# Optimization experiments

Measured on AMD Instinct MI355X. Metric: run time of the kernel, lower is better.

The kernel has to match this reference:

```python
import jax, jax.numpy as jnp
import numpy as np

B, C, H, W = 16, 256, 64, 64
HID, N, SD, NH, HD, NC = 256, 300, 64, 4, 16, 80


def _conv1x1(x, w, b):
    # x: (B,Cin,H,W), w: (Cout,Cin)
    return jnp.einsum('bchw,oc->bohw', x, w) + b[None, :, None, None]


def _lin(x, w, b):
    return x @ w.T + b


def _ln(x, g, b, eps=1e-5):
    mu = x.mean(-1, keepdims=True)
    var = ((x - mu) ** 2).mean(-1, keepdims=True)
    return (x - mu) / jnp.sqrt(var + eps) * g + b


def setup_inputs() -> dict:
    key = jax.random.key(0)
    ks = jax.random.split(key, 16)
    def w(k, shape, s=0.02):
        return jax.random.normal(k, shape, jnp.float32) * s
    return {
        'x': jax.random.normal(ks[0], (B, C, H, W), jnp.float32),
        'spotlight_sources': w(ks[1], (N, SD)),
        'pos_w': w(ks[2], (HID // 2, 2)), 'pos_b': jnp.zeros((HID // 2,), jnp.float32),
        'fp_w': w(ks[3], (HID, C)), 'fp_b': jnp.zeros((HID,), jnp.float32),
        'bn_g': jnp.ones((HID,), jnp.float32), 'bn_b': jnp.zeros((HID,), jnp.float32),
        'bn_m': jnp.zeros((HID,), jnp.float32), 'bn_v': jnp.ones((HID,), jnp.float32),
        'key_w': w(ks[4], (SD, HID)), 'key_b': jnp.zeros((SD,), jnp.float32),
        'val_w': w(ks[5], (HID, HID)), 'val_b': jnp.zeros((HID,), jnp.float32),
        'ctp_w': w(ks[6], (NC, HID)), 'ctp_b': jnp.zeros((NC,), jnp.float32),
        'bb1_w': w(ks[7], (HID, HID)), 'bb1_b': jnp.zeros((HID,), jnp.float32),
        'bbln_g': jnp.ones((HID,), jnp.float32), 'bbln_b': jnp.zeros((HID,), jnp.float32),
        'bb2_w': w(ks[8], (HID // 2, HID)), 'bb2_b': jnp.zeros((HID // 2,), jnp.float32),
        'bb3_w': w(ks[9], (4, HID // 2)), 'bb3_b': jnp.zeros((4,), jnp.float32),
        'ch1_w': w(ks[10], (HID, HID)), 'ch1_b': jnp.zeros((HID,), jnp.float32),
        'chln_g': jnp.ones((HID,), jnp.float32), 'chln_b': jnp.zeros((HID,), jnp.float32),
        'ch2_w': w(ks[11], (HID // 2, HID)), 'ch2_b': jnp.zeros((HID // 2,), jnp.float32),
        'ch3_w': w(ks[12], (1, HID // 2)), 'ch3_b': jnp.zeros((1,), jnp.float32),
    }


def _forward(x, spotlight_sources, pos_w, pos_b, fp_w, fp_b, bn_g, bn_b, bn_m, bn_v,
             key_w, key_b, val_w, val_b, ctp_w, ctp_b,
             bb1_w, bb1_b, bbln_g, bbln_b, bb2_w, bb2_b, bb3_w, bb3_b,
             ch1_w, ch1_b, chln_g, chln_b, ch2_w, ch2_b, ch3_w, ch3_b):
    Bv, _, Hh, Ww = x.shape
    # position encoding: 2-channel normalized (y, x) grid, conv1x1 to HID//2
    y = jnp.linspace(-1.0, 1.0, Hh, dtype=jnp.float32)
    xc = jnp.linspace(-1.0, 1.0, Ww, dtype=jnp.float32)
    coords = jnp.stack([jnp.broadcast_to(y[:, None], (Hh, Ww)),
                        jnp.broadcast_to(xc[None, :], (Hh, Ww))], 0)[None]  # (1,2,H,W)
    # feature_proj: conv1x1 + BatchNorm(eval) + ReLU
    feats = _conv1x1(x, fp_w, fp_b)
    feats = (feats - bn_m[None, :, None, None]) / jnp.sqrt(bn_v[None, :, None, None] + 1e-5)
    feats = jax.nn.relu(feats * bn_g[None, :, None, None] + bn_b[None, :, None, None])
    pos = jnp.broadcast_to(_conv1x1(coords, pos_w, pos_b), (Bv, HID // 2, Hh, Ww))
    comb = jnp.concatenate([feats[:, :HID // 2], pos], axis=1)  # (B,HID,H,W)
    keys = _conv1x1(comb, key_w, key_b).reshape(Bv, NH, HD, Hh * Ww)   # (B,h,d,M)
    vals = _conv1x1(comb, val_w, val_b).reshape(Bv, HID, Hh * Ww)      # (B,HID,M)
    q = spotlight_sources.reshape(N, NH, HD)                            # (N,h,d)
    logits = jnp.einsum('nhd,bhdm->bhnm', q, keys) / jnp.sqrt(jnp.float32(HD))
    attn = jax.nn.softmax(logits, axis=-1).mean(axis=1)                 # (B,N,M), head-averaged
    maps = attn.reshape(Bv, N, Hh, Ww)
    sf = jnp.einsum('bnm,bcm->bnc', attn, vals)                         # (B,N,HID)
    def head(z, w1, b1, g, bb, w2, b2, w3, b3):
        z = jax.nn.relu(_ln(_lin(z, w1, b1), g, bb))
        z = jax.nn.relu(_lin(z, w2, b2))
        return _lin(z, w3, b3)
    boxes = head(sf, bb1_w, bb1_b, bbln_g, bbln_b, bb2_w, bb2_b, bb3_w, bb3_b)
    scores = jax.nn.sigmoid(head(sf, ch1_w, ch1_b, chln_g, chln_b, ch2_w, ch2_b, ch3_w, ch3_b))
    cls = _lin(sf, ctp_w, ctp_b)
    # diversity loss: mean off-diagonal cosine similarity of attention rows
    an = attn / jnp.maximum(jnp.linalg.norm(attn, axis=2, keepdims=True), 1e-12)
    sim = jnp.einsum('bnm,bkm->bnk', an, an)
    div = (sim.sum() - jnp.einsum('bnn->', sim)) / (N * (N - 1)) * 0.1
    return boxes, scores, cls, maps, div, sf


def reference(x, spotlight_sources, pos_w, pos_b, fp_w, fp_b, bn_g, bn_b, bn_m, bn_v,
              key_w, key_b, val_w, val_b, ctp_w, ctp_b,
              bb1_w, bb1_b, bbln_g, bbln_b, bb2_w, bb2_b, bb3_w, bb3_b,
              ch1_w, ch1_b, chln_g, chln_b, ch2_w, ch2_b, ch3_w, ch3_b):
    return _forward(x, spotlight_sources, pos_w, pos_b, fp_w, fp_b, bn_g, bn_b, bn_m, bn_v,
                    key_w, key_b, val_w, val_b, ctp_w, ctp_b,
                    bb1_w, bb1_b, bbln_g, bbln_b, bb2_w, bb2_b, bb3_w, bb3_b,
                    ch1_w, ch1_b, chln_g, chln_b, ch2_w, ch2_b, ch3_w, ch3_b)
```

## Files before the change

kernel.cpp:

```cpp
#include <hip/hip_runtime.h>
#include <math.h>

#define BB 16
#define CIN 256
#define MM 4096
#define HIDC 256
#define NQ 300
#define NHH 4
#define HDD 16

#define OFF_BOXES  0
#define OFF_SCORES 19200
#define OFF_CLS    24000
#define OFF_MAPS   408000
#define OFF_DIV    20068800
#define OFF_SF     20068801

#define WS_COMB16  0
#define WS_KEYS16  8388608
#define WS_ATTN16  10485760
#define WS_T32     20316160
#define WS_T16     21544960
#define WS_VALW16  22159360
#define WS_SUMS    22192128
#define WS_NORM    22211328
#define WS_ACC     22216128
#define WS_P       22216192

#define HP_SF16   (WS_P + 0)
#define HP_Z1PRE  (WS_P + 614400)
#define HP_Z1_16  (WS_P + 1843200)
#define HP_Z2BB   (WS_P + 2457600)
#define HP_Z2CH   (WS_P + 2764800)
#define HP_HW     (WS_P + 3072000)
#define WS_Q16    (WS_P + 3200000)
#define WS_XT     25426432
#define WS_COMBT  33815040
#define WS_FPW16  42203648
#define WS_KEYW16 42220032

#define HW_BB1 0
#define HW_CH1 65536
#define HW_BB2 131072
#define HW_CH2 163840
#define HW_CTP 196608

typedef short short8 __attribute__((ext_vector_type(8)));
typedef float floatx4 __attribute__((ext_vector_type(4)));

__device__ __forceinline__ unsigned short f2bf(float f){
  unsigned int u = __float_as_uint(f);
  u = (u + 0x7FFFu + ((u >> 16) & 1u)) >> 16;
  return (unsigned short)u;
}
__device__ __forceinline__ float bf1(unsigned short u){
  return __uint_as_float((unsigned int)u << 16);
}

__global__ void zero_kernel(float* p){ p[0] = 0.f; }

__global__ __launch_bounds__(256) void zero4_kernel(float4* __restrict__ p, int n4){
  int i = blockIdx.x * 256 + threadIdx.x;
  if (i < n4) p[i] = make_float4(0.f, 0.f, 0.f, 0.f);
}

__global__ __launch_bounds__(256) void cast4_bf16_kernel(const float* __restrict__ src,
                                                         unsigned short* __restrict__ dst, int n4){
  int i = blockIdx.x * 256 + threadIdx.x;
  if (i < n4){
    float4 v = ((const float4*)src)[i];
    ushort4 u;
    u.x = f2bf(v.x); u.y = f2bf(v.y); u.z = f2bf(v.z); u.w = f2bf(v.w);
    ((ushort4*)dst)[i] = u;
  }
}

__global__ __launch_bounds__(256) void castq_kernel(const float* __restrict__ ss,
                                                    unsigned short* __restrict__ q16){
  int i = blockIdx.x * 256 + threadIdx.x;
  if (i < 320*64)
    q16[i] = (i < NQ*64) ? f2bf(ss[i] * 0.25f) : (unsigned short)0;
}

__global__ __launch_bounds__(256) void cast_w2_kernel(const float* __restrict__ fp_w,
    const float* __restrict__ key_w,
    unsigned short* __restrict__ fpw16, unsigned short* __restrict__ keyw16){
  int i = blockIdx.x * 256 + threadIdx.x;
  if (i < 128*256) fpw16[i] = f2bf(fp_w[i]);
  if (i < 64*256)  keyw16[i] = f2bf(key_w[i]);
}

__global__ __launch_bounds__(256) void cast_heads_kernel(
    const float* __restrict__ val_w, const float* __restrict__ bb1_w,
    const float* __restrict__ ch1_w, const float* __restrict__ bb2_w,
    const float* __restrict__ ch2_w, const float* __restrict__ ctp_w,
    unsigned short* __restrict__ valw16, unsigned short* __restrict__ hw16){
  int i = blockIdx.x * 256 + threadIdx.x;
  int T = gridDim.x * 256;
  for (int j = i; j < 65536; j += T) valw16[j] = f2bf(val_w[j]);
  for (int j = i; j < 65536; j += T) hw16[HW_BB1 + j] = f2bf(bb1_w[j]);
  for (int j = i; j < 65536; j += T) hw16[HW_CH1 + j] = f2bf(ch1_w[j]);
  for (int j = i; j < 32768; j += T) hw16[HW_BB2 + j] = f2bf(bb2_w[j]);
  for (int j = i; j < 32768; j += T) hw16[HW_CH2 + j] = f2bf(ch2_w[j]);
  for (int j = i; j < 20480; j += T) hw16[HW_CTP + j] = f2bf(ctp_w[j]);
}

__global__ __launch_bounds__(256) void pos_fill_kernel(const float* __restrict__ pos_w,
                                                       const float* __restrict__ pos_b,
                                                       unsigned short* __restrict__ comb16){
  int idx = blockIdx.x * 256 + threadIdx.x;
  int c = idx >> 12;
  int m = idx & 4095;
  int row = m >> 6, col = m & 63;
  float y = -1.f + 2.f * (float)row / 63.f;
  float x = -1.f + 2.f * (float)col / 63.f;
  unsigned short v = f2bf(pos_w[c*2] * y + pos_w[c*2+1] * x + pos_b[c]);
  #pragma unroll
  for (int b = 0; b < BB; b++)
    comb16[((size_t)(b*HIDC + 128 + c))*MM + m] = v;
}

template<bool INF32>
__global__ __launch_bounds__(256) void transpose_kernel(
    const void* __restrict__ in, unsigned short* __restrict__ outp){
  int b = blockIdx.z;
  int m0 = blockIdx.x * 64;
  int r0 = blockIdx.y * 64;
  __shared__ unsigned short lds[64][65];
  int t = threadIdx.x;
  if (INF32){
    const float* ib = (const float*)in + (size_t)b * CIN * MM;
    #pragma unroll
    for (int j = 0; j < 4; j++){
      int lin = j*256 + t;
      int rr = lin >> 4;
      int m4 = (lin & 15) * 4;
      float4 v = *(const float4*)&ib[(size_t)(r0 + rr)*MM + m0 + m4];
      lds[m4+0][rr] = f2bf(v.x);
      lds[m4+1][rr] = f2bf(v.y);
      lds[m4+2][rr] = f2bf(v.z);
      lds[m4+3][rr] = f2bf(v.w);
    }
  } else {
    const unsigned short* ib = (const unsigned short*)in + (size_t)b * CIN * MM;
    #pragma unroll
    for (int j = 0; j < 4; j++){
      int lin = j*256 + t;
      int rr = lin >> 4;
      int m4 = (lin & 15) * 4;
      ushort4 v = *(const ushort4*)&ib[(size_t)(r0 + rr)*MM + m0 + m4];
      lds[m4+0][rr] = v.x; lds[m4+1][rr] = v.y;
      lds[m4+2][rr] = v.z; lds[m4+3][rr] = v.w;
    }
  }
  __syncthreads();
  unsigned short* ob = outp + (size_t)b * MM * CIN;
  #pragma unroll
  for (int j = 0; j < 4; j++){
    int lin = j*256 + t;
    int mm = lin >> 4;
    int c4 = (lin & 15) * 4;
    ushort4 u;
    u.x = lds[mm][c4+0]; u.y = lds[mm][c4+1];
    u.z = lds[mm][c4+2]; u.w = lds[mm][c4+3];
    *(ushort4*)&ob[(size_t)(m0 + mm)*CIN + r0 + c4] = u;
  }
}

__global__ __launch_bounds__(64) void comb_mfma_kernel(
    const unsigned short* __restrict__ fpw16, const unsigned short* __restrict__ xT16,
    const float* __restrict__ fp_b, const float* __restrict__ bn_g,
    const float* __restrict__ bn_b, const float* __restrict__ bn_m,
    const float* __restrict__ bn_v, unsigned short* __restrict__ comb16){
  int b = blockIdx.z;
  const unsigned short* Bb = xT16 + (size_t)b * MM * CIN;
  unsigned short* cb = comb16 + (size_t)b * HIDC * MM;
  int lane = threadIdx.x;
  int r16 = lane & 15;
  int ko  = (lane >> 4) * 8;
  const unsigned short* arow[4];
  const unsigned short* brow[4];
  #pragma unroll
  for (int i = 0; i < 4; i++){
    arow[i] = fpw16 + (size_t)(blockIdx.y*64 + i*16 + r16) * CIN + ko;
    brow[i] = Bb + (size_t)(blockIdx.x*64 + i*16 + r16) * CIN + ko;
  }
  floatx4 acc[4][4];
  #pragma unroll
  for (int i = 0; i < 4; i++)
    #pragma unroll
    for (int j = 0; j < 4; j++)
      acc[i][j] = (floatx4){0.f, 0.f, 0.f, 0.f};
  short8 a[4], bv[4], a2[4], b2[4];
  #pragma unroll
  for (int i = 0; i < 4; i++){
    a[i]  = *(const short8*)(arow[i]);
    bv[i] = *(const short8*)(brow[i]);
  }
  for (int k = 32; k < CIN; k += 32){
    #pragma unroll
    for (int i = 0; i < 4; i++){
      a2[i] = *(const short8*)(arow[i] + k);
      b2[i] = *(const short8*)(brow[i] + k);
    }
    #pragma unroll
    for (int i = 0; i < 4; i++)
      #pragma unroll
      for (int j = 0; j < 4; j++)
        acc[i][j] = __builtin_amdgcn_mfma_f32_16x16x32_bf16(a[i], bv[j], acc[i][j], 0, 0, 0);
    #pragma unroll
    for (int i = 0; i < 4; i++){ a[i] = a2[i]; bv[i] = b2[i]; }
  }
  #pragma unroll
  for (int i = 0; i < 4; i++)
    #pragma unroll
    for (int j = 0; j < 4; j++)
      acc[i][j] = __builtin_amdgcn_mfma_f32_16x16x32_bf16(a[i], bv[j], acc[i][j], 0, 0, 0);
  int cq = lane & 15, rq = (lane >> 4) * 4;
  #pragma unroll
  for (int i = 0; i < 4; i++){
    #pragma unroll
    for (int reg = 0; reg < 4; reg++){
      int rr = blockIdx.y*64 + i*16 + rq + reg;
      float sc  = rsqrtf(bn_v[rr] + 1e-5f);
      float mul = sc * bn_g[rr];
      float ofs = (fp_b[rr] - bn_m[rr]) * mul + bn_b[rr];
      #pragma unroll
      for (int j = 0; j < 4; j++){
        int cc = blockIdx.x*64 + j*16 + cq;
        float v = fmaxf(acc[i][j][reg] * mul + ofs, 0.f);
        cb[(size_t)rr * MM + cc] = f2bf(v);
      }
    }
  }
}


__global__ __launch_bounds__(256) void attn_sums_kernel(
    const unsigned short* __restrict__ q16, const unsigned short* __restrict__ keysT,
    float* __restrict__ sums){
  int b = blockIdx.z, ny = blockIdx.y, mx = blockIdx.x;
  int tid = threadIdx.x, w = tid >> 6, lane = tid & 63;
  int n0 = ny * 64;
  int l15 = lane & 15, qh = lane >> 4;
  int ko = (qh & 1) * 8;
  bool lo = lane < 32;
  const unsigned short* kT = keysT + (size_t)b * MM * 64;
  int mwb = mx*512 + w*128;
  __shared__ float spart[4][NHH][64];
  short8 zz = {0,0,0,0,0,0,0,0};
  for (int h = 0; h < NHH; h++){
    short8 a[4];
    #pragma unroll
    for (int i = 0; i < 4; i++)
      a[i] = lo ? *(const short8*)&q16[(size_t)(n0 + i*16 + l15)*64 + h*16 + ko] : zz;
    floatx4 sacc[4];
    #pragma unroll
    for (int i = 0; i < 4; i++) sacc[i] = (floatx4){0.f,0.f,0.f,0.f};
    for (int ms = 0; ms < 8; ms++){
      int m = mwb + ms*16 + l15;
      short8 bf = lo ? *(const short8*)&kT[(size_t)m*64 + h*16 + ko] : zz;
      #pragma unroll
      for (int i = 0; i < 4; i++){
        floatx4 l = __builtin_amdgcn_mfma_f32_16x16x32_bf16(a[i], bf,
                        (floatx4){0.f,0.f,0.f,0.f}, 0, 0, 0);
        sacc[i][0] += __expf(l[0]); sacc[i][1] += __expf(l[1]);
        sacc[i][2] += __expf(l[2]); sacc[i][3] += __expf(l[3]);
      }
    }
    #pragma unroll
    for (int i = 0; i < 4; i++)
      #pragma unroll
      for (int reg = 0; reg < 4; reg++){
        float v = sacc[i][reg];
        v += __shfl_xor(v, 1); v += __shfl_xor(v, 2);
        v += __shfl_xor(v, 4); v += __shfl_xor(v, 8);
        if (l15 == 0) spart[w][h][i*16 + qh*4 + reg] = v;
      }
  }
  __syncthreads();
  if (tid < NHH*64){
    int h = tid >> 6, r = tid & 63, n = n0 + r;
    if (n < NQ){
      float v = spart[0][h][r] + spart[1][h][r] + spart[2][h][r] + spart[3][h][r];
      atomicAdd(&sums[((size_t)b*NHH + h)*NQ + n], v);
    }
  }
}

__global__ __launch_bounds__(256) void attn_emit_kernel(
    const unsigned short* __restrict__ q16, const unsigned short* __restrict__ keysT,
    const float* __restrict__ sums, float* __restrict__ maps,
    unsigned short* __restrict__ attn16, float* __restrict__ norms){
  int b = blockIdx.z, ny = blockIdx.y, mx = blockIdx.x;
  int tid = threadIdx.x, w = tid >> 6, lane = tid & 63;
  int n0 = ny * 64;
  int l15 = lane & 15, qh = lane >> 4;
  int ko = (qh & 1) * 8;
  int rq = qh * 4;
  bool lo = lane < 32;
  __shared__ __align__(16) float inv_s[NHH][64];
  __shared__ float npart[4][64];
  if (tid < NHH*64){
    int h = tid >> 6, r = tid & 63, n = n0 + r;
    inv_s[h][r] = (n < NQ) ? 0.25f / sums[((size_t)b*NHH + h)*NQ + n] : 0.f;
  }
  __syncthreads();
  const unsigned short* kT = keysT + (size_t)b * MM * 64;
  int mwb = mx*512 + w*128;
  short8 zz = {0,0,0,0,0,0,0,0};
  short8 a[NHH][4];
  #pragma unroll
  for (int h = 0; h < NHH; h++)
    #pragma unroll
    for (int i = 0; i < 4; i++)
      a[h][i] = lo ? *(const short8*)&q16[(size_t)(n0 + i*16 + l15)*64 + h*16 + ko] : zz;
  floatx4 nacc[4];
  #pragma unroll
  for (int i = 0; i < 4; i++) nacc[i] = (floatx4){0.f,0.f,0.f,0.f};
  float* mb = maps + (size_t)b * NQ * MM;
  unsigned short* ab = attn16 + (size_t)b * NQ * MM;
  for (int ms = 0; ms < 8; ms++){
    int m = mwb + ms*16 + l15;
    floatx4 o[4];
    #pragma unroll
    for (int i = 0; i < 4; i++) o[i] = (floatx4){0.f,0.f,0.f,0.f};
    #pragma unroll
    for (int h = 0; h < NHH; h++){
      short8 bf = lo ? *(const short8*)&kT[(size_t)m*64 + h*16 + ko] : zz;
      #pragma unroll
      for (int i = 0; i < 4; i++){
        floatx4 l = __builtin_amdgcn_mfma_f32_16x16x32_bf16(a[h][i], bf,
                        (floatx4){0.f,0.f,0.f,0.f}, 0, 0, 0);
        floatx4 iv = *(const floatx4*)&inv_s[h][i*16 + rq];
        o[i][0] += __expf(l[0]) * iv[0];
        o[i][1] += __expf(l[1]) * iv[1];
        o[i][2] += __expf(l[2]) * iv[2];
        o[i][3] += __expf(l[3]) * iv[3];
      }
    }
    #pragma unroll
    for (int i = 0; i < 4; i++){
      nacc[i][0] += o[i][0]*o[i][0]; nacc[i][1] += o[i][1]*o[i][1];
      nacc[i][2] += o[i][2]*o[i][2]; nacc[i][3] += o[i][3]*o[i][3];
      #pragma unroll
      for (int reg = 0; reg < 4; reg++){
        int n = n0 + i*16 + rq + reg;
        if (n < NQ){
          mb[(size_t)n*MM + m] = o[i][reg];
          ab[(size_t)n*MM + m] = f2bf(o[i][reg]);
        }
      }
    }
  }
  #pragma unroll
  for (int i = 0; i < 4; i++)
    #pragma unroll
    for (int reg = 0; reg < 4; reg++){
      float v = nacc[i][reg];
      v += __shfl_xor(v, 1); v += __shfl_xor(v, 2);
      v += __shfl_xor(v, 4); v += __shfl_xor(v, 8);
      if (l15 == 0) npart[w][i*16 + rq + reg] = v;
    }
  __syncthreads();
  if (tid < 64){
    int n = n0 + tid;
    if (n < NQ){
      float v = npart[0][tid] + npart[1][tid] + npart[2][tid] + npart[3][tid];
      atomicAdd(&norms[(size_t)b*NQ + n], v);
    }
  }
}

template<bool RELU>
__global__ __launch_bounds__(64) void mfma_nt_kernel(
    const unsigned short* __restrict__ A, size_t sA,
    const unsigned short* __restrict__ B, size_t sB,
    const float* __restrict__ bias,
    float* __restrict__ C, unsigned short* __restrict__ C16,
    size_t sC, int ldc, int Mr, int Nc, int K){
  int bz = blockIdx.z;
  const unsigned short* Ab = A + (size_t)bz * sA;
  const unsigned short* Bb = B + (size_t)bz * sB;
  int lane = threadIdx.x;
  int r16 = lane & 15;
  int ko  = (lane >> 4) * 8;
  const unsigned short* arow[4];
  const unsigned short* brow[4];
  #pragma unroll
  for (int i = 0; i < 4; i++){
    int m = blockIdx.y*64 + i*16 + r16;
    if (m > Mr - 1) m = Mr - 1;
    arow[i] = Ab + (size_t)m * K + ko;
    int n = blockIdx.x*64 + i*16 + r16;
    if (n > Nc - 1) n = Nc - 1;
    brow[i] = Bb + (size_t)n * K + ko;
  }
  floatx4 acc[4][4];
  #pragma unroll
  for (int i = 0; i < 4; i++)
    #pragma unroll
    for (int j = 0; j < 4; j++)
      acc[i][j] = (floatx4){0.f, 0.f, 0.f, 0.f};
  short8 a[4], bv[4], a2[4], b2[4];
  #pragma unroll
  for (int i = 0; i < 4; i++){
    a[i]  = *(const short8*)(arow[i]);
    bv[i] = *(const short8*)(brow[i]);
  }
  for (int k = 32; k < K; k += 32){
    #pragma unroll
    for (int i = 0; i < 4; i++){
      a2[i] = *(const short8*)(arow[i] + k);
      b2[i] = *(const short8*)(brow[i] + k);
    }
    #pragma unroll
    for (int i = 0; i < 4; i++)
      #pragma unroll
      for (int j = 0; j < 4; j++)
        acc[i][j] = __builtin_amdgcn_mfma_f32_16x16x32_bf16(a[i], bv[j], acc[i][j], 0, 0, 0);
    #pragma unroll
    for (int i = 0; i < 4; i++){ a[i] = a2[i]; bv[i] = b2[i]; }
  }
  #pragma unroll
  for (int i = 0; i < 4; i++)
    #pragma unroll
    for (int j = 0; j < 4; j++)
      acc[i][j] = __builtin_amdgcn_mfma_f32_16x16x32_bf16(a[i], bv[j], acc[i][j], 0, 0, 0);
  int cq = lane & 15, rq = (lane >> 4) * 4;
  #pragma unroll
  for (int j = 0; j < 4; j++){
    int cc = blockIdx.x*64 + j*16 + cq;
    if (cc >= Nc) continue;
    float bv_ = bias ? bias[cc] : 0.f;
    #pragma unroll
    for (int i = 0; i < 4; i++){
      int rbase = blockIdx.y*64 + i*16 + rq;
      #pragma unroll
      for (int reg = 0; reg < 4; reg++){
        int rr = rbase + reg;
        if (rr < Mr){
          float v = acc[i][j][reg] + bv_;
          if (RELU) v = fmaxf(v, 0.f);
          size_t o = (size_t)bz * sC + (size_t)rr * ldc + cc;
          if (C)   C[o] = v;
          if (C16) C16[o] = f2bf(v);
        }
      }
    }
  }
}

__global__ __launch_bounds__(64) void mfma_nt_splitk_kernel(
    const unsigned short* __restrict__ A, size_t sA,
    const unsigned short* __restrict__ B, size_t sB,
    float* __restrict__ C, size_t sC, int ldc, int Mr, int K, int kchunk){
  int nks = K / kchunk;
  int bz = blockIdx.z / nks;
  int kz = blockIdx.z % nks;
  const unsigned short* Ab = A + (size_t)bz * sA + (size_t)kz * kchunk;
  const unsigned short* Bb = B + (size_t)bz * sB + (size_t)kz * kchunk;
  int lane = threadIdx.x;
  int r16 = lane & 15;
  int ko  = (lane >> 4) * 8;
  const unsigned short* arow[4];
  const unsigned short* brow[4];
  #pragma unroll
  for (int i = 0; i < 4; i++){
    int m = blockIdx.y*64 + i*16 + r16;
    if (m > Mr - 1) m = Mr - 1;
    arow[i] = Ab + (size_t)m * K + ko;
    int n = blockIdx.x*64 + i*16 + r16;
    brow[i] = Bb + (size_t)n * K + ko;
  }
  floatx4 acc[4][4];
  #pragma unroll
  for (int i = 0; i < 4; i++)
    #pragma unroll
    for (int j = 0; j < 4; j++)
      acc[i][j] = (floatx4){0.f, 0.f, 0.f, 0.f};
  short8 a[4], bv[4], a2[4], b2[4];
  #pragma unroll
  for (int i = 0; i < 4; i++){
    a[i]  = *(const short8*)(arow[i]);
    bv[i] = *(const short8*)(brow[i]);
  }
  for (int k = 32; k < kchunk; k += 32){
    #pragma unroll
    for (int i = 0; i < 4; i++){
      a2[i] = *(const short8*)(arow[i] + k);
      b2[i] = *(const short8*)(brow[i] + k);
    }
    #pragma unroll
    for (int i = 0; i < 4; i++)
      #pragma unroll
      for (int j = 0; j < 4; j++)
        acc[i][j] = __builtin_amdgcn_mfma_f32_16x16x32_bf16(a[i], bv[j], acc[i][j], 0, 0, 0);
    #pragma unroll
    for (int i = 0; i < 4; i++){ a[i] = a2[i]; bv[i] = b2[i]; }
  }
  #pragma unroll
  for (int i = 0; i < 4; i++)
    #pragma unroll
    for (int j = 0; j < 4; j++)
      acc[i][j] = __builtin_amdgcn_mfma_f32_16x16x32_bf16(a[i], bv[j], acc[i][j], 0, 0, 0);
  int cq = lane & 15, rq = (lane >> 4) * 4;
  #pragma unroll
  for (int j = 0; j < 4; j++){
    int cc = blockIdx.x*64 + j*16 + cq;
    #pragma unroll
    for (int i = 0; i < 4; i++){
      int rbase = blockIdx.y*64 + i*16 + rq;
      #pragma unroll
      for (int reg = 0; reg < 4; reg++){
        int rr = rbase + reg;
        if (rr < Mr)
          atomicAdd(&C[(size_t)bz * sC + (size_t)rr * ldc + cc], acc[i][j][reg]);
      }
    }
  }
}

__global__ __launch_bounds__(256) void ln_relu_kernel(const float* __restrict__ zin,
    const float* __restrict__ g, const float* __restrict__ bvec,
    unsigned short* __restrict__ zout){
  int row = blockIdx.x * 4 + (threadIdx.x >> 6);
  int lane = threadIdx.x & 63;
  float4 v = *(const float4*)&zin[(size_t)row * 256 + lane * 4];
  float s = v.x + v.y + v.z + v.w;
  #pragma unroll
  for (int off = 32; off >= 1; off >>= 1) s += __shfl_xor(s, off);
  float mean = s * (1.f/256.f);
  float dx = v.x - mean, dy = v.y - mean, dz = v.z - mean, dw = v.w - mean;
  float sq = dx*dx + dy*dy + dz*dz + dw*dw;
  #pragma unroll
  for (int off = 32; off >= 1; off >>= 1) sq += __shfl_xor(sq, off);
  float inv = rsqrtf(sq * (1.f/256.f) + 1e-5f);
  float4 gv = *(const float4*)&g[lane * 4];
  float4 bb = *(const float4*)&bvec[lane * 4];
  ushort4 u;
  u.x = f2bf(fmaxf(dx*inv*gv.x + bb.x, 0.f));
  u.y = f2bf(fmaxf(dy*inv*gv.y + bb.y, 0.f));
  u.z = f2bf(fmaxf(dz*inv*gv.z + bb.z, 0.f));
  u.w = f2bf(fmaxf(dw*inv*gv.w + bb.w, 0.f));
  *(ushort4*)&zout[(size_t)row * 256 + lane * 4] = u;
}

__global__ __launch_bounds__(256) void head3_kernel(
    const unsigned short* __restrict__ z2bb, const unsigned short* __restrict__ z2ch,
    const float* __restrict__ bb3_w, const float* __restrict__ bb3_b,
    const float* __restrict__ ch3_w, const float* __restrict__ ch3_b,
    float* __restrict__ boxes, float* __restrict__ scores){
  int row = blockIdx.x * 4 + (threadIdx.x >> 6);
  int lane = threadIdx.x & 63;
  float zb0 = bf1(z2bb[(size_t)row*128 + 2*lane]);
  float zb1 = bf1(z2bb[(size_t)row*128 + 2*lane + 1]);
  float zc0 = bf1(z2ch[(size_t)row*128 + 2*lane]);
  float zc1 = bf1(z2ch[(size_t)row*128 + 2*lane + 1]);
  float acc[5];
  #pragma unroll
  for (int o = 0; o < 4; o++)
    acc[o] = bb3_w[o*128 + 2*lane]*zb0 + bb3_w[o*128 + 2*lane + 1]*zb1;
  acc[4] = ch3_w[2*lane]*zc0 + ch3_w[2*lane + 1]*zc1;
  #pragma unroll
  for (int o = 0; o < 5; o++){
    float v = acc[o];
    #pragma unroll
    for (int off = 32; off >= 1; off >>= 1) v += __shfl_xor(v, off);
    acc[o] = v;
  }
  if (lane == 0){
    #pragma unroll
    for (int o = 0; o < 4; o++)
      boxes[(size_t)row*4 + o] = acc[o] + bb3_b[o];
    float sv = acc[4] + ch3_b[0];
    scores[row] = 1.f / (1.f + __expf(-sv));
  }
}

__global__ __launch_bounds__(256) void simdiv_kernel(const unsigned short* __restrict__ attn16,
    const float* __restrict__ norms, float* __restrict__ acc){
  int b = blockIdx.y;
  int m = blockIdx.x * 256 + threadIdx.x;
  __shared__ float inv_s[NQ];
  __shared__ float red[4];
  for (int i = threadIdx.x; i < NQ; i += 256)
    inv_s[i] = 1.f / fmaxf(sqrtf(norms[(size_t)b * NQ + i]), 1e-12f);
  __syncthreads();
  const unsigned short* ab = attn16 + (size_t)b * NQ * MM;
  float S = 0.f;
  for (int n = 0; n < NQ; n++)
    S += bf1(ab[(size_t)n * MM + m]) * inv_s[n];
  float p = S * S;
  #pragma unroll
  for (int off = 32; off >= 1; off >>= 1) p += __shfl_xor(p, off);
  int w = threadIdx.x >> 6, lane = threadIdx.x & 63;
  if (lane == 0) red[w] = p;
  __syncthreads();
  if (threadIdx.x == 0) atomicAdd(acc, red[0] + red[1] + red[2] + red[3]);
}

__global__ void finalize_kernel(const float* __restrict__ acc, float* __restrict__ out_div){
  out_div[0] = (acc[0] - (float)(BB * NQ)) / (float)(NQ * (NQ - 1)) * 0.1f;
}

extern "C" void kernel_launch(void* const* d_in, const int* in_sizes, int n_in,
                              void* d_out, int out_size, void* d_ws, size_t ws_size,
                              hipStream_t stream){
  const float* x      = (const float*)d_in[0];
  const float* ss     = (const float*)d_in[1];
  const float* pos_w  = (const float*)d_in[2];
  const float* pos_b  = (const float*)d_in[3];
  const float* fp_w   = (const float*)d_in[4];
  const float* fp_b   = (const float*)d_in[5];
  const float* bn_g   = (const float*)d_in[6];
  const float* bn_b   = (const float*)d_in[7];
  const float* bn_m   = (const float*)d_in[8];
  const float* bn_v   = (const float*)d_in[9];
  const float* key_w  = (const float*)d_in[10];
  const float* key_b  = (const float*)d_in[11];
  const float* val_w  = (const float*)d_in[12];
  const float* val_b  = (const float*)d_in[13];
  const float* ctp_w  = (const float*)d_in[14];
  const float* ctp_b  = (const float*)d_in[15];
  const float* bb1_w  = (const float*)d_in[16];
  const float* bb1_b  = (const float*)d_in[17];
  const float* bbln_g = (const float*)d_in[18];
  const float* bbln_b = (const float*)d_in[19];
  const float* bb2_w  = (const float*)d_in[20];
  const float* bb2_b  = (const float*)d_in[21];
  const float* bb3_w  = (const float*)d_in[22];
  const float* bb3_b  = (const float*)d_in[23];
  const float* ch1_w  = (const float*)d_in[24];
  const float* ch1_b  = (const float*)d_in[25];
  const float* chln_g = (const float*)d_in[26];
  const float* chln_b = (const float*)d_in[27];
  const float* ch2_w  = (const float*)d_in[28];
  const float* ch2_b  = (const float*)d_in[29];
  const float* ch3_w  = (const float*)d_in[30];
  const float* ch3_b  = (const float*)d_in[31];

  float* out    = (float*)d_out;
  float* boxes  = out + OFF_BOXES;
  float* scores = out + OFF_SCORES;
  float* cls    = out + OFF_CLS;
  float* maps   = out + OFF_MAPS;
  float* divp   = out + OFF_DIV;
  float* sfout  = out + OFF_SF;

  float* ws = (float*)d_ws;
  unsigned short* comb16 = (unsigned short*)(ws + WS_COMB16);
  unsigned short* keysT  = (unsigned short*)(ws + WS_KEYS16);
  unsigned short* attn16 = (unsigned short*)(ws + WS_ATTN16);
  float*          t32    = ws + WS_T32;
  unsigned short* t16    = (unsigned short*)(ws + WS_T16);
  unsigned short* valw16 = (unsigned short*)(ws + WS_VALW16);
  float* sums  = ws + WS_SUMS;
  float* norms = ws + WS_NORM;
  float* dacc  = ws + WS_ACC;
  unsigned short* sf16   = (unsigned short*)(ws + HP_SF16);
  float*          z1pre  = ws + HP_Z1PRE;
  unsigned short* z1_16  = (unsigned short*)(ws + HP_Z1_16);
  unsigned short* z2bb16 = (unsigned short*)(ws + HP_Z2BB);
  unsigned short* z2ch16 = (unsigned short*)(ws + HP_Z2CH);
  unsigned short* hw16   = (unsigned short*)(ws + HP_HW);
  unsigned short* q16    = (unsigned short*)(ws + WS_Q16);
  unsigned short* xT16   = (unsigned short*)(ws + WS_XT);
  unsigned short* combT  = (unsigned short*)(ws + WS_COMBT);
  unsigned short* fpw16  = (unsigned short*)(ws + WS_FPW16);
  unsigned short* keyw16 = (unsigned short*)(ws + WS_KEYW16);

  zero_kernel<<<1, 1, 0, stream>>>(dacc);
  zero4_kernel<<<1200, 256, 0, stream>>>((float4*)t32, 307200);
  zero4_kernel<<<24, 256, 0, stream>>>((float4*)sums, 6000);
  castq_kernel<<<80, 256, 0, stream>>>(ss, q16);
  cast_w2_kernel<<<128, 256, 0, stream>>>(fp_w, key_w, fpw16, keyw16);

  transpose_kernel<true><<<dim3(64,4,16), 256, 0, stream>>>(x, xT16);
  pos_fill_kernel<<<2048, 256, 0, stream>>>(pos_w, pos_b, comb16);
  comb_mfma_kernel<<<dim3(64,2,16), 64, 0, stream>>>(
      fpw16, xT16, fp_b, bn_g, bn_b, bn_m, bn_v, comb16);
  transpose_kernel<false><<<dim3(64,4,16), 256, 0, stream>>>(comb16, combT);
  mfma_nt_kernel<false><<<dim3(1,64,16), 64, 0, stream>>>(
      combT, (size_t)MM*CIN, keyw16, 0, key_b,
      nullptr, keysT, (size_t)MM*64, 64, MM, 64, CIN);

  attn_sums_kernel<<<dim3(8,5,16), 256, 0, stream>>>(q16, keysT, sums);
  attn_emit_kernel<<<dim3(8,5,16), 256, 0, stream>>>(q16, keysT, sums, maps, attn16, norms);

  mfma_nt_splitk_kernel<<<dim3(4,5,BB*4), 64, 0, stream>>>(
      attn16, (size_t)NQ*MM, comb16, (size_t)HIDC*MM,
      t32, (size_t)NQ*HIDC, HIDC, NQ, MM, MM/4);
  cast4_bf16_kernel<<<1200, 256, 0, stream>>>(t32, t16, 307200);
  cast_heads_kernel<<<256, 256, 0, stream>>>(val_w, bb1_w, ch1_w, bb2_w, ch2_w, ctp_w, valw16, hw16);
  mfma_nt_kernel<false><<<dim3(4,5,BB), 64, 0, stream>>>(
      t16, (size_t)NQ*HIDC, valw16, 0, val_b,
      sfout, sf16, (size_t)NQ*HIDC, HIDC, NQ, HIDC, HIDC);

  mfma_nt_kernel<false><<<dim3(4,75,1), 64, 0, stream>>>(
      sf16, 0, hw16 + HW_BB1, 0, bb1_b, z1pre, nullptr, 0, 256, 4800, 256, 256);
  ln_relu_kernel<<<1200, 256, 0, stream>>>(z1pre, bbln_g, bbln_b, z1_16);
  mfma_nt_kernel<true><<<dim3(2,75,1), 64, 0, stream>>>(
      z1_16, 0, hw16 + HW_BB2, 0, bb2_b, nullptr, z2bb16, 0, 128, 4800, 128, 256);
  mfma_nt_kernel<false><<<dim3(4,75,1), 64, 0, stream>>>(
      sf16, 0, hw16 + HW_CH1, 0, ch1_b, z1pre, nullptr, 0, 256, 4800, 256, 256);
  ln_relu_kernel<<<1200, 256, 0, stream>>>(z1pre, chln_g, chln_b, z1_16);
  mfma_nt_kernel<true><<<dim3(2,75,1), 64, 0, stream>>>(
      z1_16, 0, hw16 + HW_CH2, 0, ch2_b, nullptr, z2ch16, 0, 128, 4800, 128, 256);
  head3_kernel<<<1200, 256, 0, stream>>>(z2bb16, z2ch16, bb3_w, bb3_b, ch3_w, ch3_b, boxes, scores);
  mfma_nt_kernel<false><<<dim3(2,75,1), 64, 0, stream>>>(
      sf16, 0, hw16 + HW_CTP, 0, ctp_b, cls, nullptr, 0, 80, 4800, 80, 256);

  simdiv_kernel<<<dim3(16,16), 256, 0, stream>>>(attn16, norms, dacc);
  finalize_kernel<<<1, 1, 0, stream>>>(dacc, divp);
}
```

Measured before the change: 565.2 us.

## Coalesce attention map stores via LDS staging, write positional channels transposed directly

The attention emit kernel now stages each 64x16 tile of outputs in shared memory and writes maps and attn16 as float4/ushort4 rows instead of scattered scalar stores. The positional-embedding half of the transposed combined features is filled directly by a new kernel, so the comb transpose only covers the first 128 channels. Both attention kernels use a finer split over positions (twice as many blocks, with the position loop unrolled) for more parallelism, and the transpose LDS row padding changes. The trade-offs are extra LDS use and a barrier-free staging step per wave, plus one extra kernel launch.

```diff
diff --git a/kernel.cpp b/kernel.cpp
--- a/kernel.cpp
+++ b/kernel.cpp
@@ -120,13 +120,32 @@
     comb16[((size_t)(b*HIDC + 128 + c))*MM + m] = v;
 }
 
+__global__ __launch_bounds__(256) void pos_fillT_kernel(const float* __restrict__ pos_w,
+                                                        const float* __restrict__ pos_b,
+                                                        unsigned short* __restrict__ combT){
+  int lin = blockIdx.x * 256 + threadIdx.x;
+  int c4 = (lin & 31) * 4;
+  int m  = lin >> 5;
+  int row = m >> 6, col = m & 63;
+  float y = -1.f + 2.f * (float)row / 63.f;
+  float x = -1.f + 2.f * (float)col / 63.f;
+  ushort4 u;
+  u.x = f2bf(pos_w[(c4+0)*2] * y + pos_w[(c4+0)*2+1] * x + pos_b[c4+0]);
+  u.y = f2bf(pos_w[(c4+1)*2] * y + pos_w[(c4+1)*2+1] * x + pos_b[c4+1]);
+  u.z = f2bf(pos_w[(c4+2)*2] * y + pos_w[(c4+2)*2+1] * x + pos_b[c4+2]);
+  u.w = f2bf(pos_w[(c4+3)*2] * y + pos_w[(c4+3)*2+1] * x + pos_b[c4+3]);
+  #pragma unroll
+  for (int b = 0; b < BB; b++)
+    *(ushort4*)&combT[((size_t)b*MM + m)*CIN + 128 + c4] = u;
+}
+
 template<bool INF32>
 __global__ __launch_bounds__(256) void transpose_kernel(
     const void* __restrict__ in, unsigned short* __restrict__ outp){
   int b = blockIdx.z;
   int m0 = blockIdx.x * 64;
   int r0 = blockIdx.y * 64;
-  __shared__ unsigned short lds[64][65];
+  __shared__ unsigned short lds[64][68];
   int t = threadIdx.x;
   if (INF32){
     const float* ib = (const float*)in + (size_t)b * CIN * MM;
@@ -246,7 +265,7 @@
   int ko = (qh & 1) * 8;
   bool lo = lane < 32;
   const unsigned short* kT = keysT + (size_t)b * MM * 64;
-  int mwb = mx*512 + w*128;
+  int mwb = mx*256 + w*64;
   __shared__ float spart[4][NHH][64];
   short8 zz = {0,0,0,0,0,0,0,0};
   for (int h = 0; h < NHH; h++){
@@ -257,7 +276,8 @@
     floatx4 sacc[4];
     #pragma unroll
     for (int i = 0; i < 4; i++) sacc[i] = (floatx4){0.f,0.f,0.f,0.f};
-    for (int ms = 0; ms < 8; ms++){
+    #pragma unroll
+    for (int ms = 0; ms < 4; ms++){
       int m = mwb + ms*16 + l15;
       short8 bf = lo ? *(const short8*)&kT[(size_t)m*64 + h*16 + ko] : zz;
       #pragma unroll
@@ -301,13 +321,14 @@
   bool lo = lane < 32;
   __shared__ __align__(16) float inv_s[NHH][64];
   __shared__ float npart[4][64];
+  __shared__ __align__(16) float tbuf[4][64][20];
   if (tid < NHH*64){
     int h = tid >> 6, r = tid & 63, n = n0 + r;
     inv_s[h][r] = (n < NQ) ? 0.25f / sums[((size_t)b*NHH + h)*NQ + n] : 0.f;
   }
   __syncthreads();
   const unsigned short* kT = keysT + (size_t)b * MM * 64;
-  int mwb = mx*512 + w*128;
+  int mwb = mx*256 + w*64;
   short8 zz = {0,0,0,0,0,0,0,0};
   short8 a[NHH][4];
   #pragma unroll
@@ -320,8 +341,10 @@
   for (int i = 0; i < 4; i++) nacc[i] = (floatx4){0.f,0.f,0.f,0.f};
   float* mb = maps + (size_t)b * NQ * MM;
   unsigned short* ab = attn16 + (size_t)b * NQ * MM;
-  for (int ms = 0; ms < 8; ms++){
-    int m = mwb + ms*16 + l15;
+  #pragma unroll
+  for (int ms = 0; ms < 4; ms++){
+    int mbase = mwb + ms*16;
+    int m = mbase + l15;
     floatx4 o[4];
     #pragma unroll
     for (int i = 0; i < 4; i++) o[i] = (floatx4){0.f,0.f,0.f,0.f};
@@ -344,12 +367,20 @@
       nacc[i][0] += o[i][0]*o[i][0]; nacc[i][1] += o[i][1]*o[i][1];
       nacc[i][2] += o[i][2]*o[i][2]; nacc[i][3] += o[i][3]*o[i][3];
       #pragma unroll
-      for (int reg = 0; reg < 4; reg++){
-        int n = n0 + i*16 + rq + reg;
-        if (n < NQ){
-          mb[(size_t)n*MM + m] = o[i][reg];
-          ab[(size_t)n*MM + m] = f2bf(o[i][reg]);
-        }
+      for (int reg = 0; reg < 4; reg++)
+        tbuf[w][i*16 + rq + reg][l15] = o[i][reg];
+    }
+    #pragma unroll
+    for (int pass = 0; pass < 4; pass++){
+      int row = pass*16 + (lane >> 2);
+      int n = n0 + row;
+      float4 v = *(const float4*)&tbuf[w][row][(lane & 3) * 4];
+      if (n < NQ){
+        size_t off = (size_t)n*MM + mbase + (lane & 3)*4;
+        *(float4*)&mb[off] = v;
+        ushort4 u;
+        u.x = f2bf(v.x); u.y = f2bf(v.y); u.z = f2bf(v.z); u.w = f2bf(v.w);
+        *(ushort4*)&ab[off] = u;
       }
     }
   }
@@ -678,15 +709,16 @@
 
   transpose_kernel<true><<<dim3(64,4,16), 256, 0, stream>>>(x, xT16);
   pos_fill_kernel<<<2048, 256, 0, stream>>>(pos_w, pos_b, comb16);
+  pos_fillT_kernel<<<512, 256, 0, stream>>>(pos_w, pos_b, combT);
   comb_mfma_kernel<<<dim3(64,2,16), 64, 0, stream>>>(
       fpw16, xT16, fp_b, bn_g, bn_b, bn_m, bn_v, comb16);
-  transpose_kernel<false><<<dim3(64,4,16), 256, 0, stream>>>(comb16, combT);
+  transpose_kernel<false><<<dim3(64,2,16), 256, 0, stream>>>(comb16, combT);
   mfma_nt_kernel<false><<<dim3(1,64,16), 64, 0, stream>>>(
       combT, (size_t)MM*CIN, keyw16, 0, key_b,
       nullptr, keysT, (size_t)MM*64, 64, MM, 64, CIN);
 
-  attn_sums_kernel<<<dim3(8,5,16), 256, 0, stream>>>(q16, keysT, sums);
-  attn_emit_kernel<<<dim3(8,5,16), 256, 0, stream>>>(q16, keysT, sums, maps, attn16, norms);
+  attn_sums_kernel<<<dim3(16,5,16), 256, 0, stream>>>(q16, keysT, sums);
+  attn_emit_kernel<<<dim3(16,5,16), 256, 0, stream>>>(q16, keysT, sums, maps, attn16, norms);
 
   mfma_nt_splitk_kernel<<<dim3(4,5,BB*4), 64, 0, stream>>>(
       attn16, (size_t)NQ*MM, comb16, (size_t)HIDC*MM,
```

After: 582.7 us. 1.03x slower.
